# Kernel optimization log

Hardware: AMD Instinct MI355X
Metric: run time of the kernel (lower is better)

## Reference

```python
import jax, jax.numpy as jnp
import numpy as np

B = 2048       # batch
POOL = 512     # e_prompt_pool_size
TOPK = 4       # top_k
EPL = 8        # e_prompt_length
GPL = 8        # g_prompt_length
EMB = 768      # emb_d
KEYD = 768     # key_dim


def setup_inputs() -> dict:
    key = jax.random.key(0)
    k1, k2, k3, k4, k5 = jax.random.split(key, 5)
    return {
        "x_querry": jax.random.normal(k1, (B, KEYD), dtype=jnp.float32),
        "x_block": jax.random.normal(k2, (B, EMB), dtype=jnp.float32),
        "e_k": jax.random.uniform(k3, (POOL, KEYD), dtype=jnp.float32),
        "e_p": jax.random.uniform(k4, (POOL, EPL, EMB), dtype=jnp.float32),
        "g_p": jax.random.uniform(k5, (GPL, EMB), dtype=jnp.float32),
        "l": 0,
    }


def _l2norm(x, eps=1e-12):
    # matches torch F.normalize(dim=-1): x / max(||x||, eps)
    n = jnp.sqrt(jnp.sum(x * x, axis=-1, keepdims=True))
    return x / jnp.maximum(n, eps)


def reference(x_querry, x_block, e_k, e_p, g_p, l):
    # ---- E-prompt routing (l in e_layers) ----
    n_K = _l2norm(e_k)                              # [P, C]
    q = jax.lax.stop_gradient(_l2norm(x_querry))    # [B, C], detached in torch
    cos_sim = jnp.einsum('bj,kj->bk', q, n_K)       # [B, P]
    distance = 1.0 - cos_sim
    # use_contrastiv=False -> mass = 1.0
    scaled_distance = distance * 1.0
    # torch.topk(largest=False) == top_k of negated values
    _, k_idx = jax.lax.top_k(-scaled_distance, TOPK)   # [B, K]
    P_ = e_p[k_idx]                                  # [B, K, EPL, EMB] gather
    # non-contrastive loss: (1 - cos_sim[:, k_idx]).mean() -> [B, B, K] mean
    loss = jnp.mean(1.0 - cos_sim[:, k_idx])
    i = EPL // 2
    Ek = P_[:, :, :i, :].reshape(B, -1, EMB)         # [B, K*i, EMB]
    Ev = P_[:, :, i:, :].reshape(B, -1, EMB)
    # count scatter (train_count update)
    counts = jnp.bincount(k_idx.reshape(-1), length=POOL)

    # ---- G-prompt (l in g_layers) ----
    j = GPL // 2
    Gk = jnp.broadcast_to(g_p[:j], (B, j, EMB))
    Gv = jnp.broadcast_to(g_p[j:], (B, GPL - j, EMB))

    Pk = jnp.concatenate([Ek, Gk], axis=1)           # [B, K*i + j, EMB]
    Pv = jnp.concatenate([Ev, Gv], axis=1)
    return Pk, Pv, loss, counts, x_block
```

## Files before the change

kernel.cpp:

```cpp
#include <hip/hip_runtime.h>
#include <math.h>

static constexpr int NB    = 2048;
static constexpr int NPOOL = 512;
static constexpr int NTOPK = 4;
static constexpr int NEPL  = 8;
static constexpr int NEMB  = 768;
static constexpr int NSLOT = 20;

__global__ __launch_bounds__(256) void norms_kernel(
    const float* __restrict__ xq, const float* __restrict__ ek,
    double* __restrict__ qinv, double* __restrict__ kinv,
    float* __restrict__ rqn, float* __restrict__ rkn,
    double* __restrict__ u, double* __restrict__ lacc,
    int* __restrict__ done, int* __restrict__ counts) {
  int row = blockIdx.x;
  if (row == NB + NPOOL) {
    for (int i = threadIdx.x; i < NEMB; i += 256) u[i] = 0.0;
    for (int i = threadIdx.x; i < NPOOL; i += 256) counts[i] = 0;
    if (threadIdx.x == 0) { *lacc = 0.0; *done = 0; }
    return;
  }
  const float* src;
  double* dinv;
  float* rdst;
  if (row < NB) { src = xq + (size_t)row * NEMB; dinv = qinv + row; rdst = rqn + row; }
  else          { src = ek + (size_t)(row - NB) * NEMB; dinv = kinv + (row - NB); rdst = rkn + (row - NB); }
  double s = 0.0;
  for (int i = threadIdx.x; i < NEMB; i += 256) {
    double v = (double)src[i];
    s += v * v;
  }
  for (int off = 32; off > 0; off >>= 1) s += __shfl_down(s, off, 64);
  __shared__ double red[4];
  if ((threadIdx.x & 63) == 0) red[threadIdx.x >> 6] = s;
  __syncthreads();
  if (threadIdx.x == 0) {
    double n = sqrt(red[0] + red[1] + red[2] + red[3]);
    double inv = 1.0 / fmax(n, 1e-12);
    *dinv = inv;
    *rdst = (float)inv;
  }
}

__global__ __launch_bounds__(256) void cos_kernel(
    const float* __restrict__ xq, const float* __restrict__ ek,
    const float* __restrict__ rqn, const float* __restrict__ rkn,
    const double* __restrict__ qinv, float* __restrict__ cosm,
    double* __restrict__ u) {
  if (blockIdx.x >= NPOOL / 64) {
    int b = (blockIdx.x - NPOOL / 64) * (NB / 64) + blockIdx.y;
    int c0 = threadIdx.x;
    int r0 = b * 32;
    double s0 = 0.0, s1 = 0.0, s2 = 0.0;
    for (int r = r0; r < r0 + 32; r++) {
      double inv = qinv[r];
      const float* xr = xq + (size_t)r * NEMB;
      s0 = fma((double)xr[c0], inv, s0);
      s1 = fma((double)xr[c0 + 256], inv, s1);
      s2 = fma((double)xr[c0 + 512], inv, s2);
    }
    atomicAdd(&u[c0], s0);
    atomicAdd(&u[c0 + 256], s1);
    atomicAdd(&u[c0 + 512], s2);
    return;
  }
  __shared__ float As[32][68];
  __shared__ float Bs[32][68];
  const int t = threadIdx.x;
  const int tx = t & 15;
  const int ty = t >> 4;
  const int bp = blockIdx.x * 64;
  const int bb = blockIdx.y * 64;
  float acc[4][4] = {};
  for (int k0 = 0; k0 < NEMB; k0 += 32) {
#pragma unroll
    for (int uu = 0; uu < 2; uu++) {
      int uidx = t + uu * 256;
      int m = uidx >> 3;
      int k4 = (uidx & 7) * 4;
      float4 a = *(const float4*)(xq + (size_t)(bb + m) * NEMB + k0 + k4);
      float4 bvv = *(const float4*)(ek + (size_t)(bp + m) * NEMB + k0 + k4);
      As[k4 + 0][m] = a.x; As[k4 + 1][m] = a.y; As[k4 + 2][m] = a.z; As[k4 + 3][m] = a.w;
      Bs[k4 + 0][m] = bvv.x; Bs[k4 + 1][m] = bvv.y; Bs[k4 + 2][m] = bvv.z; Bs[k4 + 3][m] = bvv.w;
    }
    __syncthreads();
#pragma unroll
    for (int kk = 0; kk < 32; kk++) {
      float4 av = *(const float4*)&As[kk][ty * 4];
      float4 bv = *(const float4*)&Bs[kk][tx * 4];
      acc[0][0] = fmaf(av.x, bv.x, acc[0][0]); acc[0][1] = fmaf(av.x, bv.y, acc[0][1]);
      acc[0][2] = fmaf(av.x, bv.z, acc[0][2]); acc[0][3] = fmaf(av.x, bv.w, acc[0][3]);
      acc[1][0] = fmaf(av.y, bv.x, acc[1][0]); acc[1][1] = fmaf(av.y, bv.y, acc[1][1]);
      acc[1][2] = fmaf(av.y, bv.z, acc[1][2]); acc[1][3] = fmaf(av.y, bv.w, acc[1][3]);
      acc[2][0] = fmaf(av.z, bv.x, acc[2][0]); acc[2][1] = fmaf(av.z, bv.y, acc[2][1]);
      acc[2][2] = fmaf(av.z, bv.z, acc[2][2]); acc[2][3] = fmaf(av.z, bv.w, acc[2][3]);
      acc[3][0] = fmaf(av.w, bv.x, acc[3][0]); acc[3][1] = fmaf(av.w, bv.y, acc[3][1]);
      acc[3][2] = fmaf(av.w, bv.z, acc[3][2]); acc[3][3] = fmaf(av.w, bv.w, acc[3][3]);
    }
    __syncthreads();
  }
  float4 rk = *(const float4*)&rkn[bp + tx * 4];
#pragma unroll
  for (int i = 0; i < 4; i++) {
    float rq = rqn[bb + ty * 4 + i];
    float4 cv;
    cv.x = acc[i][0] * rq * rk.x;
    cv.y = acc[i][1] * rq * rk.y;
    cv.z = acc[i][2] * rq * rk.z;
    cv.w = acc[i][3] * rq * rk.w;
    *(float4*)(cosm + (size_t)(bb + ty * 4 + i) * NPOOL + bp + tx * 4) = cv;
  }
}

__device__ __forceinline__ bool btf(float av, int ai, float bv, int bi) {
  return (av > bv) || (av == bv && ai < bi);
}
__device__ __forceinline__ bool btd(double av, int ai, double bv, int bi) {
  return (av > bv) || (av == bv && ai < bi);
}
#define CE(a, b)                                                        \
  do {                                                                  \
    if (!btf(v[a], vi[a], v[b], vi[b])) {                               \
      float tv = v[a]; v[a] = v[b]; v[b] = tv;                          \
      int ti = vi[a]; vi[a] = vi[b]; vi[b] = ti;                        \
    }                                                                   \
  } while (0)

__global__ __launch_bounds__(256) void topk_gather_kernel(
    const float* __restrict__ cosm, const float* __restrict__ xq,
    const float* __restrict__ ek, const double* __restrict__ qinv,
    const double* __restrict__ kinv, const float* __restrict__ e_p,
    const float* __restrict__ g_p, const float* __restrict__ x_block,
    int* __restrict__ counts, float* __restrict__ Pk, float* __restrict__ Pv,
    float* __restrict__ out_xb) {
  const int row = blockIdx.x;
  __shared__ int sidx[4];
  const int wave = threadIdx.x >> 6, lane = threadIdx.x & 63;
  if (wave == 0) {
    const float* crow = cosm + (size_t)row * NPOOL;
    float v[8]; int vi[8];
#pragma unroll
    for (int j = 0; j < 8; j++) {
      int p = j * 64 + lane;
      v[j] = crow[p];
      vi[j] = p;
    }
    CE(0,1); CE(2,3); CE(4,5); CE(6,7);
    CE(0,2); CE(1,3); CE(4,6); CE(5,7);
    CE(1,2); CE(5,6);
    CE(0,4); CE(1,5); CE(2,6); CE(3,7);
    CE(2,4); CE(3,5);
    CE(1,2); CE(3,4); CE(5,6);
#pragma unroll
    for (int off = 1; off < 64; off <<= 1) {
      float ov[8]; int oi[8];
#pragma unroll
      for (int m = 0; m < 8; m++) {
        ov[m] = __shfl_xor(v[m], off, 64);
        oi[m] = __shfl_xor(vi[m], off, 64);
      }
#pragma unroll
      for (int m = 0; m < 8; m++) {
        if (!btf(v[m], vi[m], ov[7 - m], oi[7 - m])) { v[m] = ov[7 - m]; vi[m] = oi[7 - m]; }
      }
      CE(0,4); CE(1,5); CE(2,6); CE(3,7);
      CE(0,2); CE(1,3); CE(4,6); CE(5,7);
      CE(0,1); CE(2,3); CE(4,5); CE(6,7);
    }
    const float* xrow = xq + (size_t)row * NEMB;
    double xr[12];
#pragma unroll
    for (int e = 0; e < 12; e++) xr[e] = (double)xrow[lane * 12 + e];
    double qi = qinv[row];
    double cand[8];
#pragma unroll
    for (int c = 0; c < 8; c++) {
      int pi = vi[c];
      const float* kb = ek + (size_t)pi * NEMB + lane * 12;
      double s = 0.0;
#pragma unroll
      for (int e = 0; e < 12; e++) s = fma(xr[e], (double)kb[e], s);
#pragma unroll
      for (int off = 1; off < 64; off <<= 1) s += __shfl_xor(s, off, 64);
      cand[c] = s * qi * kinv[pi];
    }
    bool used[8] = {false, false, false, false, false, false, false, false};
#pragma unroll
    for (int m = 0; m < NTOPK; m++) {
      int best = -1;
#pragma unroll
      for (int c = 0; c < 8; c++) {
        if (!used[c] && (best < 0 || btd(cand[c], vi[c], cand[best], vi[best]))) best = c;
      }
      used[best] = true;
      if (lane == 0) {
        sidx[m] = vi[best];
        atomicAdd(&counts[vi[best]], 1);
      }
    }
  }
  __syncthreads();
  float4* dk = (float4*)(Pk + (size_t)row * NSLOT * NEMB);
  float4* dv = (float4*)(Pv + (size_t)row * NSLOT * NEMB);
  const int R = NEMB / 4;
  for (int uidx = threadIdx.x; uidx < NSLOT * R; uidx += 256) {
    int s = uidx / R;
    int r = uidx - s * R;
    const float4* sk;
    const float4* sv;
    if (s < 16) {
      int pi = sidx[s >> 2];
      int tt = s & 3;
      const float* basek = e_p + ((size_t)pi * NEPL + tt) * NEMB;
      sk = (const float4*)basek;
      sv = (const float4*)(basek + 4 * NEMB);
    } else {
      sk = (const float4*)(g_p + (size_t)(s - 16) * NEMB);
      sv = (const float4*)(g_p + (size_t)(s - 16 + 4) * NEMB);
    }
    dk[uidx] = sk[r];
    dv[uidx] = sv[r];
  }
  for (int i = threadIdx.x; i < NEMB; i += 256)
    out_xb[(size_t)row * NEMB + i] = x_block[(size_t)row * NEMB + i];
}
#undef CE

__global__ __launch_bounds__(256) void loss_kernel(
    const float* __restrict__ ek, const double* __restrict__ kinv,
    const double* __restrict__ u, const int* __restrict__ counts,
    double* __restrict__ lacc, int* __restrict__ done,
    float* __restrict__ out_loss, float* __restrict__ out_counts) {
  __shared__ double tp[NPOOL];
  for (int p = threadIdx.x; p < NPOOL; p += 256) {
    int c = counts[p];
    tp[p] = (double)c * kinv[p];
    if (blockIdx.x == 0) out_counts[p] = (float)c;
  }
  __syncthreads();
  const int j = blockIdx.x * 256 + threadIdx.x;
  double m = 0.0;
  for (int p = 0; p < NPOOL; p++) m = fma(tp[p], (double)ek[(size_t)p * NEMB + j], m);
  double part = m * u[j];
  for (int off = 32; off > 0; off >>= 1) part += __shfl_down(part, off, 64);
  __shared__ double red[4];
  if ((threadIdx.x & 63) == 0) red[threadIdx.x >> 6] = part;
  __syncthreads();
  if (threadIdx.x == 0) {
    double tot = red[0] + red[1] + red[2] + red[3];
    atomicAdd(lacc, tot);
    __threadfence();
    int d = atomicAdd(done, 1);
    if (d == 2) {
      double total = atomicAdd(lacc, 0.0);
      *out_loss = (float)(1.0 - total / (double)((long long)NB * NB * NTOPK));
    }
  }
}

extern "C" void kernel_launch(void* const* d_in, const int* in_sizes, int n_in,
                              void* d_out, int out_size, void* d_ws, size_t ws_size,
                              hipStream_t stream) {
  const float* x_querry = (const float*)d_in[0];
  const float* x_block  = (const float*)d_in[1];
  const float* e_k      = (const float*)d_in[2];
  const float* e_p      = (const float*)d_in[3];
  const float* g_p      = (const float*)d_in[4];

  double* qinv   = (double*)d_ws;
  double* kinv   = qinv + NB;
  double* u      = kinv + NPOOL;
  double* lacc   = u + NEMB;
  int*    done   = (int*)(lacc + 1);
  float*  rqn    = (float*)(done + 2);
  float*  rkn    = rqn + NB;
  float*  cosm   = rkn + NPOOL;
  int*    counts = (int*)(cosm + (size_t)NB * NPOOL);

  float* out        = (float*)d_out;
  float* Pk         = out;
  float* Pv         = Pk + (size_t)NB * NSLOT * NEMB;
  float* out_loss   = Pv + (size_t)NB * NSLOT * NEMB;
  float* out_counts = out_loss + 1;
  float* out_xb     = out_counts + NPOOL;

  norms_kernel<<<NB + NPOOL + 1, 256, 0, stream>>>(
      x_querry, e_k, qinv, kinv, rqn, rkn, u, lacc, done, counts);
  cos_kernel<<<dim3(NPOOL / 64 + 2, NB / 64), 256, 0, stream>>>(
      x_querry, e_k, rqn, rkn, qinv, cosm, u);
  topk_gather_kernel<<<NB, 256, 0, stream>>>(
      cosm, x_querry, e_k, qinv, kinv, e_p, g_p, x_block, counts, Pk, Pv, out_xb);
  loss_kernel<<<3, 256, 0, stream>>>(
      e_k, kinv, u, counts, lacc, done, out_loss, out_counts);
}
```

Measured before the change: 426.4 us.

## Split fused top-k/gather kernel into wave-per-row top-k and separate gather

New measurement: 413.7 us. 1.03x faster.

```diff
diff --git a/kernel.cpp b/kernel.cpp
--- a/kernel.cpp
+++ b/kernel.cpp
@@ -127,105 +127,117 @@
     }                                                                   \
   } while (0)
 
-__global__ __launch_bounds__(256) void topk_gather_kernel(
+__global__ __launch_bounds__(256) void topk_kernel(
     const float* __restrict__ cosm, const float* __restrict__ xq,
     const float* __restrict__ ek, const double* __restrict__ qinv,
-    const double* __restrict__ kinv, const float* __restrict__ e_p,
-    const float* __restrict__ g_p, const float* __restrict__ x_block,
-    int* __restrict__ counts, float* __restrict__ Pk, float* __restrict__ Pv,
+    const double* __restrict__ kinv, int* __restrict__ kidx,
+    int* __restrict__ counts) {
+  int wave = threadIdx.x >> 6, lane = threadIdx.x & 63;
+  int row = blockIdx.x * 4 + wave;
+  const float* crow = cosm + (size_t)row * NPOOL;
+  float v[8]; int vi[8];
+#pragma unroll
+  for (int j = 0; j < 8; j++) {
+    int p = j * 64 + lane;
+    v[j] = crow[p];
+    vi[j] = p;
+  }
+  CE(0,1); CE(2,3); CE(4,5); CE(6,7);
+  CE(0,2); CE(1,3); CE(4,6); CE(5,7);
+  CE(1,2); CE(5,6);
+  CE(0,4); CE(1,5); CE(2,6); CE(3,7);
+  CE(2,4); CE(3,5);
+  CE(1,2); CE(3,4); CE(5,6);
+#pragma unroll
+  for (int off = 1; off < 64; off <<= 1) {
+    float ov[8]; int oi[8];
+#pragma unroll
+    for (int m = 0; m < 8; m++) {
+      ov[m] = __shfl_xor(v[m], off, 64);
+      oi[m] = __shfl_xor(vi[m], off, 64);
+    }
+#pragma unroll
+    for (int m = 0; m < 8; m++) {
+      if (!btf(v[m], vi[m], ov[7 - m], oi[7 - m])) { v[m] = ov[7 - m]; vi[m] = oi[7 - m]; }
+    }
+    CE(0,4); CE(1,5); CE(2,6); CE(3,7);
+    CE(0,2); CE(1,3); CE(4,6); CE(5,7);
+    CE(0,1); CE(2,3); CE(4,5); CE(6,7);
+  }
+  const float* xrow = xq + (size_t)row * NEMB;
+  double xr[12];
+#pragma unroll
+  for (int e = 0; e < 12; e++) xr[e] = (double)xrow[lane * 12 + e];
+  double qi = qinv[row];
+  double cand[8];
+#pragma unroll
+  for (int c = 0; c < 8; c++) {
+    int pi = vi[c];
+    const float* kb = ek + (size_t)pi * NEMB + lane * 12;
+    double s = 0.0;
+#pragma unroll
+    for (int e = 0; e < 12; e++) s = fma(xr[e], (double)kb[e], s);
+#pragma unroll
+    for (int off = 1; off < 64; off <<= 1) s += __shfl_xor(s, off, 64);
+    cand[c] = s * qi * kinv[pi];
+  }
+  bool used[8] = {false, false, false, false, false, false, false, false};
+#pragma unroll
+  for (int m = 0; m < NTOPK; m++) {
+    int best = -1;
+#pragma unroll
+    for (int c = 0; c < 8; c++) {
+      if (!used[c] && (best < 0 || btd(cand[c], vi[c], cand[best], vi[best]))) best = c;
+    }
+    used[best] = true;
+    if (lane == 0) {
+      kidx[row * 4 + m] = vi[best];
+      atomicAdd(&counts[vi[best]], 1);
+    }
+  }
+}
+#undef CE
+
+__global__ __launch_bounds__(256) void gather_kernel(
+    const float* __restrict__ e_p, const float* __restrict__ g_p,
+    const int* __restrict__ kidx, const float* __restrict__ x_block,
+    float* __restrict__ Pk, float* __restrict__ Pv,
     float* __restrict__ out_xb) {
-  const int row = blockIdx.x;
-  __shared__ int sidx[4];
-  const int wave = threadIdx.x >> 6, lane = threadIdx.x & 63;
-  if (wave == 0) {
-    const float* crow = cosm + (size_t)row * NPOOL;
-    float v[8]; int vi[8];
-#pragma unroll
-    for (int j = 0; j < 8; j++) {
-      int p = j * 64 + lane;
-      v[j] = crow[p];
-      vi[j] = p;
-    }
-    CE(0,1); CE(2,3); CE(4,5); CE(6,7);
-    CE(0,2); CE(1,3); CE(4,6); CE(5,7);
-    CE(1,2); CE(5,6);
-    CE(0,4); CE(1,5); CE(2,6); CE(3,7);
-    CE(2,4); CE(3,5);
-    CE(1,2); CE(3,4); CE(5,6);
-#pragma unroll
-    for (int off = 1; off < 64; off <<= 1) {
-      float ov[8]; int oi[8];
-#pragma unroll
-      for (int m = 0; m < 8; m++) {
-        ov[m] = __shfl_xor(v[m], off, 64);
-        oi[m] = __shfl_xor(vi[m], off, 64);
-      }
-#pragma unroll
-      for (int m = 0; m < 8; m++) {
-        if (!btf(v[m], vi[m], ov[7 - m], oi[7 - m])) { v[m] = ov[7 - m]; vi[m] = oi[7 - m]; }
-      }
-      CE(0,4); CE(1,5); CE(2,6); CE(3,7);
-      CE(0,2); CE(1,3); CE(4,6); CE(5,7);
-      CE(0,1); CE(2,3); CE(4,5); CE(6,7);
-    }
-    const float* xrow = xq + (size_t)row * NEMB;
-    double xr[12];
-#pragma unroll
-    for (int e = 0; e < 12; e++) xr[e] = (double)xrow[lane * 12 + e];
-    double qi = qinv[row];
-    double cand[8];
-#pragma unroll
-    for (int c = 0; c < 8; c++) {
-      int pi = vi[c];
-      const float* kb = ek + (size_t)pi * NEMB + lane * 12;
-      double s = 0.0;
-#pragma unroll
-      for (int e = 0; e < 12; e++) s = fma(xr[e], (double)kb[e], s);
-#pragma unroll
-      for (int off = 1; off < 64; off <<= 1) s += __shfl_xor(s, off, 64);
-      cand[c] = s * qi * kinv[pi];
-    }
-    bool used[8] = {false, false, false, false, false, false, false, false};
-#pragma unroll
-    for (int m = 0; m < NTOPK; m++) {
-      int best = -1;
-#pragma unroll
-      for (int c = 0; c < 8; c++) {
-        if (!used[c] && (best < 0 || btd(cand[c], vi[c], cand[best], vi[best]))) best = c;
-      }
-      used[best] = true;
-      if (lane == 0) {
-        sidx[m] = vi[best];
-        atomicAdd(&counts[vi[best]], 1);
-      }
-    }
-  }
+  int b = blockIdx.x;
+  __shared__ int idx[4];
+  if (threadIdx.x < 4) idx[threadIdx.x] = kidx[b * 4 + threadIdx.x];
   __syncthreads();
-  float4* dk = (float4*)(Pk + (size_t)row * NSLOT * NEMB);
-  float4* dv = (float4*)(Pv + (size_t)row * NSLOT * NEMB);
+  float4* dk = (float4*)(Pk + (size_t)b * NSLOT * NEMB);
+  float4* dv = (float4*)(Pv + (size_t)b * NSLOT * NEMB);
   const int R = NEMB / 4;
-  for (int uidx = threadIdx.x; uidx < NSLOT * R; uidx += 256) {
-    int s = uidx / R;
-    int r = uidx - s * R;
+  for (int u = threadIdx.x; u < NSLOT * R; u += 256) {
+    int s = u / R;
+    int r = u - s * R;
     const float4* sk;
     const float4* sv;
     if (s < 16) {
-      int pi = sidx[s >> 2];
-      int tt = s & 3;
-      const float* basek = e_p + ((size_t)pi * NEPL + tt) * NEMB;
+      int pi = idx[s >> 2];
+      int t = s & 3;
+      const float* basek = e_p + ((size_t)pi * NEPL + t) * NEMB;
       sk = (const float4*)basek;
       sv = (const float4*)(basek + 4 * NEMB);
     } else {
       sk = (const float4*)(g_p + (size_t)(s - 16) * NEMB);
       sv = (const float4*)(g_p + (size_t)(s - 16 + 4) * NEMB);
     }
-    dk[uidx] = sk[r];
-    dv[uidx] = sv[r];
-  }
-  for (int i = threadIdx.x; i < NEMB; i += 256)
-    out_xb[(size_t)row * NEMB + i] = x_block[(size_t)row * NEMB + i];
-}
-#undef CE
+    dk[u] = sk[r];
+    dv[u] = sv[r];
+  }
+  const float* xsrc = x_block + (size_t)b * NEMB;
+  float* xdst = out_xb + (size_t)b * NEMB;
+  if (threadIdx.x < 3) xdst[threadIdx.x] = xsrc[threadIdx.x];
+  if (threadIdx.x == 3) xdst[NEMB - 1] = xsrc[NEMB - 1];
+  for (int k = threadIdx.x; k < 191; k += 256) {
+    int i = 3 + 4 * k;
+    float4 vv = make_float4(xsrc[i], xsrc[i + 1], xsrc[i + 2], xsrc[i + 3]);
+    *(float4*)(xdst + i) = vv;
+  }
+}
 
 __global__ __launch_bounds__(256) void loss_kernel(
     const float* __restrict__ ek, const double* __restrict__ kinv,
@@ -276,7 +288,8 @@
   float*  rqn    = (float*)(done + 2);
   float*  rkn    = rqn + NB;
   float*  cosm   = rkn + NPOOL;
-  int*    counts = (int*)(cosm + (size_t)NB * NPOOL);
+  int*    kidx   = (int*)(cosm + (size_t)NB * NPOOL);
+  int*    counts = kidx + NB * NTOPK;
 
   float* out        = (float*)d_out;
   float* Pk         = out;
@@ -289,8 +302,10 @@
       x_querry, e_k, qinv, kinv, rqn, rkn, u, lacc, done, counts);
   cos_kernel<<<dim3(NPOOL / 64 + 2, NB / 64), 256, 0, stream>>>(
       x_querry, e_k, rqn, rkn, qinv, cosm, u);
-  topk_gather_kernel<<<NB, 256, 0, stream>>>(
-      cosm, x_querry, e_k, qinv, kinv, e_p, g_p, x_block, counts, Pk, Pv, out_xb);
+  topk_kernel<<<NB / 4, 256, 0, stream>>>(
+      cosm, x_querry, e_k, qinv, kinv, kidx, counts);
+  gather_kernel<<<NB, 256, 0, stream>>>(
+      e_p, g_p, kidx, x_block, Pk, Pv, out_xb);
   loss_kernel<<<3, 256, 0, stream>>>(
       e_k, kinv, u, counts, lacc, done, out_loss, out_counts);
 }
```
